# Kernel optimization log

Measured on AMD Instinct MI355X. Metric: run time of the kernel, lower is better.

## Reference

```python
import jax, jax.numpy as jnp
import numpy as np

SOS_TOKEN = 1
B, H, V, T = 64, 1024, 32000, 40
INPUT_SIZE = 4096


def setup_inputs() -> dict:
    key = jax.random.key(0)
    ks = jax.random.split(key, 12)
    s = 1.0 / np.sqrt(H)
    return {
        "output": jax.random.normal(ks[0], (B, INPUT_SIZE), jnp.float32),
        "h0": jax.random.normal(ks[1], (1, B, H), jnp.float32),
        "c0": jax.random.normal(ks[2], (1, B, H), jnp.float32),
        "target_outputs": jax.random.randint(ks[3], (B, T), 0, V, jnp.int64),
        "target_lengths": jnp.full((B,), T, jnp.int64),
        "embed": jax.random.normal(ks[4], (V, H), jnp.float32),
        "w_ih": jax.random.uniform(ks[5], (4 * H, H), jnp.float32, -s, s),
        "w_hh": jax.random.uniform(ks[6], (4 * H, H), jnp.float32, -s, s),
        "b_ih": jax.random.uniform(ks[7], (4 * H,), jnp.float32, -s, s),
        "b_hh": jax.random.uniform(ks[8], (4 * H,), jnp.float32, -s, s),
        "w_out": jax.random.uniform(ks[9], (V, H), jnp.float32, -s, s),
        "b_out": jax.random.uniform(ks[10], (V,), jnp.float32, -s, s),
    }


def _lstm_cell(x, h, c, w_ih, w_hh, b_ih, b_hh):
    # PyTorch LSTMCell math; gate order i, f, g, o
    gates = x @ w_ih.T + b_ih + h @ w_hh.T + b_hh  # [B, 4H]
    i, f, g, o = jnp.split(gates, 4, axis=-1)
    c2 = jax.nn.sigmoid(f) * c + jax.nn.sigmoid(i) * jnp.tanh(g)
    h2 = jax.nn.sigmoid(o) * jnp.tanh(c2)
    return h2, c2


def reference(output, h0, c0, target_outputs, target_lengths,
              embed, w_ih, w_hh, b_ih, b_hh, w_out, b_out):
    batch = output.shape[0]
    max_lens = int(jnp.max(target_lengths))
    h, c = h0[0], c0[0]  # num_layers=1 -> [B, H]

    # Initial symbol = SOS; initial dec_o = W(embed(SOS)) (no LSTM), as in torch code
    symbol0 = jnp.full((batch,), SOS_TOKEN, dtype=target_outputs.dtype)
    dec_o0 = embed[symbol0] @ w_out.T + b_out  # [B, V]

    def step(carry, _):
        symbol, dec_o, h, c = carry
        # emit current (symbol, dec_o), then decode next
        x = embed[symbol]  # [B, H]
        h2, c2 = _lstm_cell(x, h, c, w_ih, w_hh, b_ih, b_hh)
        dec2 = h2 @ w_out.T + b_out  # [B, V]
        sym2 = jnp.argmax(dec2, axis=-1).astype(symbol.dtype)  # greedy topk(1)
        return (sym2, dec2, h2, c2), (symbol, dec_o)
    (_, _, _, _), (symbols, decs) = jax.lax.scan(
        step, (symbol0, dec_o0, h, c), None, length=max_lens)

    decoder_outs = jnp.transpose(decs, (1, 0, 2))  # [B, T, V]
    symbol_outs = jnp.transpose(symbols, (1, 0))   # [B, T]
    return decoder_outs, symbol_outs
```

## Files before the change

### kernel.cpp

```cpp
#include <hip/hip_runtime.h>

#define Bdim 64
#define Hdim 1024
#define Vdim 32000
#define Tdim 40

typedef __bf16 bf16x8 __attribute__((ext_vector_type(8)));
typedef float  f32x4  __attribute__((ext_vector_type(4)));
typedef unsigned short u16x8 __attribute__((ext_vector_type(8)));
static_assert(sizeof(bf16x8) == 16, "bf16x8 must be 16B");

__device__ __forceinline__ unsigned long long pack_key(float f, int v) {
    unsigned u = __float_as_uint(f);
    u = (u & 0x80000000u) ? ~u : (u | 0x80000000u);
    return ((unsigned long long)u << 32) | (unsigned long long)(0xFFFFFFFFu - (unsigned)v);
}

__device__ __forceinline__ int decode_key(unsigned long long key) {
    return (int)(0xFFFFFFFFu - (unsigned)(key & 0xFFFFFFFFull));
}

__device__ __forceinline__ void gll16(const void* g, void* l) {
    __builtin_amdgcn_global_load_lds(
        (const __attribute__((address_space(1))) void*)g,
        (__attribute__((address_space(3))) void*)l, 16, 0, 0);
}

struct BSplit2 { unsigned short h, m; };

__device__ __forceinline__ BSplit2 bsplit2v(float x) {
    __bf16 h = (__bf16)x;  float r = x - (float)h;
    __bf16 m = (__bf16)r;
    BSplit2 s;
    s.h = __builtin_bit_cast(unsigned short, h);
    s.m = __builtin_bit_cast(unsigned short, m);
    return s;
}

__device__ __forceinline__ void bsplit2(float x, unsigned short& a, unsigned short& b) {
    BSplit2 s = bsplit2v(x);
    a = s.h; b = s.m;
}

template<int NW, int NCH, bool ARGMAX, bool BIAS, bool GATHER, bool NTST>
__device__ __forceinline__ void mm_core(
    unsigned char* sm,
    unsigned long long (*red)[4][16],
    const float* __restrict__ W,
    const unsigned short* __restrict__ Ah,
    const unsigned short* __restrict__ Am,
    const float* __restrict__ Gsrc,
    const unsigned long long* __restrict__ slots_in, int tstep,
    float* __restrict__ sym_dst,
    int n0, const float* __restrict__ bias,
    float* __restrict__ out, size_t out_bstride,
    unsigned long long* __restrict__ slots_out)
{
    constexpr int NT     = NW * 64;
    constexpr int WBYTES = NW * 2048;
    constexpr int BUFSZ  = WBYTES + 8192;

    const int tid  = threadIdx.x;
    const int lane = tid & 63;
    const int wid  = tid >> 6;

    f32x4 acc[4] = {};

    const unsigned char* Wb = (const unsigned char*)W;
    const unsigned char* Apb[2] = {(const unsigned char*)Ah, (const unsigned char*)Am};

    const int ar = tid >> 2, as = tid & 3;
    const int aswz = as ^ ((ar >> 1) & 3);
    const size_t asrc_off = (size_t)ar * 2048 + (size_t)aswz * 16;
    const size_t aldst    = (size_t)ar * 64 + (size_t)aswz * 16;

    const float* grow = nullptr;
    if constexpr (GATHER) {
        if (tid < 256) {
            int symv = 1;
            if (tstep > 0) {
                unsigned long long key = slots_in[ar];
                symv = decode_key(key);
                if (sym_dst != nullptr && as == 0)
                    sym_dst[ar * Tdim + tstep] = (float)symv;
            }
            grow = Gsrc + (size_t)symv * 1024 + as * 8;
        }
    }

    auto stage = [&](int bufidx, int ch) {
        unsigned char* bb = sm + bufidx * BUFSZ;
        const size_t kb4 = (size_t)ch * 128;
#pragma unroll
        for (int s = 0; s < 2; s++) {
            int gg = tid + NT * s;
            int rw = gg >> 3, cc = gg & 7;
            int sg = cc ^ (rw & 7);
            gll16(Wb + (size_t)rw * 4096 + kb4 + (size_t)sg * 16,
                  bb + ((wid * 64 + NT * s) << 4));
        }
        if constexpr (GATHER) {
            if (tid < 256) {
                const float* p = grow + ch * 32;
                float4 f0 = *(const float4*)(p);
                float4 f1 = *(const float4*)(p + 4);
                u16x8 vh, vm;
                BSplit2 s0 = bsplit2v(f0.x); vh[0] = s0.h; vm[0] = s0.m;
                BSplit2 s1 = bsplit2v(f0.y); vh[1] = s1.h; vm[1] = s1.m;
                BSplit2 s2 = bsplit2v(f0.z); vh[2] = s2.h; vm[2] = s2.m;
                BSplit2 s3 = bsplit2v(f0.w); vh[3] = s3.h; vm[3] = s3.m;
                BSplit2 s4 = bsplit2v(f1.x); vh[4] = s4.h; vm[4] = s4.m;
                BSplit2 s5 = bsplit2v(f1.y); vh[5] = s5.h; vm[5] = s5.m;
                BSplit2 s6 = bsplit2v(f1.z); vh[6] = s6.h; vm[6] = s6.m;
                BSplit2 s7 = bsplit2v(f1.w); vh[7] = s7.h; vm[7] = s7.m;
                *(u16x8*)(bb + WBYTES + aldst)        = vh;
                *(u16x8*)(bb + WBYTES + 4096 + aldst) = vm;
            }
        } else {
            if (tid < 256) {
                const size_t kb2 = (size_t)ch * 64;
#pragma unroll
                for (int pl = 0; pl < 2; pl++)
                    gll16(Apb[pl] + asrc_off + kb2,
                          bb + WBYTES + pl * 4096 + (wid << 10));
            }
        }
    };

    stage(0, 0);
    __syncthreads();

    const int col  = lane & 15;
    const int kg   = lane >> 4;
    const int wrow = wid * 16 + col;
    const int wg0  = (2 * kg) ^ (wrow & 7);
    const int wg1  = (2 * kg + 1) ^ (wrow & 7);

#pragma unroll 2
    for (int ch = 0; ch < NCH; ch++) {
        if (ch + 1 < NCH) stage((ch + 1) & 1, ch + 1);
        unsigned char* base = sm + (ch & 1) * BUFSZ;

        const unsigned char* Wr = base + wrow * 128;
        f32x4 w0 = *(const f32x4*)(Wr + (wg0 << 4));
        f32x4 w1 = *(const f32x4*)(Wr + (wg1 << 4));
        bf16x8 whi, wmid;
#pragma unroll
        for (int j = 0; j < 4; j++) {
            float x0 = w0[j], x1 = w1[j];
            __bf16 a0 = (__bf16)x0; float r0 = x0 - (float)a0;
            whi[j] = a0; wmid[j] = (__bf16)r0;
            __bf16 a1 = (__bf16)x1; float r1 = x1 - (float)a1;
            whi[4 + j] = a1; wmid[4 + j] = (__bf16)r1;
        }
#pragma unroll
        for (int bt = 0; bt < 4; bt++) {
            const int arow = bt * 16 + col;
            const unsigned char* Ar = base + WBYTES + arow * 64
                                    + ((kg ^ ((arow >> 1) & 3)) << 4);
            bf16x8 ahi = *(const bf16x8*)Ar;
            bf16x8 ami = *(const bf16x8*)(Ar + 4096);
            acc[bt] = __builtin_amdgcn_mfma_f32_16x16x32_bf16(whi,  ahi, acc[bt], 0, 0, 0);
            acc[bt] = __builtin_amdgcn_mfma_f32_16x16x32_bf16(whi,  ami, acc[bt], 0, 0, 0);
            acc[bt] = __builtin_amdgcn_mfma_f32_16x16x32_bf16(wmid, ahi, acc[bt], 0, 0, 0);
        }
        __syncthreads();
    }

    const int ncol = n0 + wid * 16 + kg * 4;
    f32x4 bv = {};
    if (BIAS) bv = *(const f32x4*)(bias + ncol);

    unsigned long long bk[4];
#pragma unroll
    for (int bt = 0; bt < 4; bt++) {
        const int b = bt * 16 + col;
        float* op = out + (size_t)b * out_bstride + ncol;
        f32x4 vv;
        unsigned long long best = 0ull;
#pragma unroll
        for (int r = 0; r < 4; r++) {
            float val = acc[bt][r];
            if (BIAS) val += bv[r];
            vv[r] = val;
            if (ARGMAX) {
                unsigned long long key = pack_key(val, ncol + r);
                if (key > best) best = key;
            }
        }
        if constexpr (NTST)
            __builtin_nontemporal_store(vv, (f32x4*)op);
        else
            *(f32x4*)op = vv;
        bk[bt] = best;
    }

    if constexpr (ARGMAX) {
#pragma unroll
        for (int bt = 0; bt < 4; bt++) {
            unsigned long long k = bk[bt];
            unsigned long long o = __shfl_xor(k, 16, 64); if (o > k) k = o;
            o = __shfl_xor(k, 32, 64);                    if (o > k) k = o;
            if (lane < 16) red[wid][bt][lane] = k;
        }
        __syncthreads();
        if (tid < 64) {
            const int bt = tid >> 4, c = tid & 15;
            unsigned long long k = red[0][bt][c];
#pragma unroll
            for (int w = 1; w < NW; w++)
                if (red[w][bt][c] > k) k = red[w][bt][c];
            atomicMax(&slots_out[bt * 16 + c], k);
        }
    }
}

template<bool AM>
__global__ __launch_bounds__(512, 1) void k_logits(
    const float* __restrict__ w_out,
    const unsigned short* __restrict__ ah, const unsigned short* __restrict__ am,
    const float* __restrict__ b_out, float* __restrict__ out,
    unsigned long long* __restrict__ slots)
{
    __shared__ __align__(16) unsigned char smem[2][24576];
    __shared__ unsigned long long red[8][4][16];
    const int vb = blockIdx.x * 128;
    mm_core<8, 32, AM, true, false, true>(&smem[0][0], red,
        w_out + (size_t)vb * Hdim, ah, am, nullptr, nullptr, 0, nullptr,
        vb, b_out, out, (size_t)Tdim * Vdim, slots);
}

__global__ __launch_bounds__(256, 2) void k_gates(
    const float* __restrict__ w_ih, const float* __restrict__ w_hh,
    const unsigned short* __restrict__ hh, const unsigned short* __restrict__ hm,
    const float* __restrict__ embed, unsigned long long* __restrict__ slots,
    int t, float* __restrict__ sym_out, float* __restrict__ gp)
{
    __shared__ __align__(16) unsigned char smem[2][16384];
    const int nbi = blockIdx.x, y = blockIdx.y, z = blockIdx.z;
    const float* W = (y ? w_hh : w_ih) + (size_t)nbi * 65536 + z * 256;
    float* gout = gp + (size_t)(y * 4 + z) * (Bdim * 4096);
    if (y)
        mm_core<4, 8, false, false, false, false>(&smem[0][0], nullptr, W,
            hh + z * 256, hm + z * 256, nullptr, nullptr, t, nullptr,
            nbi * 64, nullptr, gout, 4096, nullptr);
    else
        mm_core<4, 8, false, false, true, false>(&smem[0][0], nullptr, W,
            nullptr, nullptr, embed + z * 256, slots, t,
            ((nbi == 0 && z == 0) ? sym_out : nullptr),
            nbi * 64, nullptr, gout, 4096, nullptr);
}

__global__ void k_cell(const float* __restrict__ gp, const float* __restrict__ b_ih,
                       const float* __restrict__ b_hh, float* __restrict__ cbuf,
                       unsigned short* __restrict__ hh, unsigned short* __restrict__ hm,
                       unsigned long long* __restrict__ slots)
{
    const int idx = blockIdx.x * 256 + threadIdx.x;
    const int b = idx >> 10, k = idx & 1023;
    const size_t S = (size_t)Bdim * 4096;
    const size_t base = (size_t)b * 4096;
    float g[4];
#pragma unroll
    for (int q = 0; q < 4; q++) {
        size_t o = base + q * 1024 + k;
        float s = gp[o];
#pragma unroll
        for (int i = 1; i < 8; i++) s += gp[i * S + o];
        g[q] = s + b_ih[q * 1024 + k] + b_hh[q * 1024 + k];
    }
    float si = 1.f / (1.f + expf(-g[0]));
    float sf = 1.f / (1.f + expf(-g[1]));
    float so = 1.f / (1.f + expf(-g[3]));
    float c  = cbuf[idx];
    float c2 = sf * c + si * tanhf(g[2]);
    float h2 = so * tanhf(c2);
    cbuf[idx] = c2;
    unsigned short hs, ms;
    bsplit2(h2, hs, ms);
    const size_t o = (size_t)b * 1024 + k;
    hh[o] = hs; hm[o] = ms;
    if (idx < 64) slots[idx] = 0ull;
}

__global__ void k_init(const float* __restrict__ embed, const float* __restrict__ h0,
                       const float* __restrict__ c0,
                       unsigned short* __restrict__ xsh, unsigned short* __restrict__ xsm,
                       unsigned short* __restrict__ hh, unsigned short* __restrict__ hm,
                       float* __restrict__ cbuf, float* __restrict__ sym_out,
                       unsigned long long* __restrict__ slots)
{
    const int b = blockIdx.x, t4 = threadIdx.x * 4;
    if (threadIdx.x == 0) { sym_out[b * Tdim] = 1.0f; slots[b] = 0ull; }
    const size_t o = (size_t)b * 1024 + t4;
    ushort4 hi4, mi4;

    float4 e = *(const float4*)(embed + 1024 + t4);
    bsplit2(e.x, hi4.x, mi4.x);
    bsplit2(e.y, hi4.y, mi4.y);
    bsplit2(e.z, hi4.z, mi4.z);
    bsplit2(e.w, hi4.w, mi4.w);
    *(ushort4*)(xsh + o) = hi4; *(ushort4*)(xsm + o) = mi4;

    float4 hv = *(const float4*)(h0 + (size_t)b * 1024 + t4);
    bsplit2(hv.x, hi4.x, mi4.x);
    bsplit2(hv.y, hi4.y, mi4.y);
    bsplit2(hv.z, hi4.z, mi4.z);
    bsplit2(hv.w, hi4.w, mi4.w);
    *(ushort4*)(hh + o) = hi4; *(ushort4*)(hm + o) = mi4;

    float4 cv = *(const float4*)(c0 + (size_t)b * 1024 + t4);
    *(float4*)(cbuf + (size_t)b * 1024 + t4) = cv;
}

__global__ void k_symfinal(const unsigned long long* __restrict__ slots,
                           float* __restrict__ sym_out)
{
    const int b = threadIdx.x;
    sym_out[b * Tdim + (Tdim - 1)] = (float)decode_key(slots[b]);
}

extern "C" void kernel_launch(void* const* d_in, const int* in_sizes, int n_in,
                              void* d_out, int out_size, void* d_ws, size_t ws_size,
                              hipStream_t stream)
{
    const float* h0    = (const float*)d_in[1];
    const float* c0    = (const float*)d_in[2];
    const float* embed = (const float*)d_in[5];
    const float* w_ih  = (const float*)d_in[6];
    const float* w_hh  = (const float*)d_in[7];
    const float* b_ih  = (const float*)d_in[8];
    const float* b_hh  = (const float*)d_in[9];
    const float* w_out = (const float*)d_in[10];
    const float* b_out = (const float*)d_in[11];

    float* out = (float*)d_out;
    float* sym_out = out + (size_t)Bdim * Tdim * Vdim;

    unsigned short* hh  = (unsigned short*)d_ws;
    unsigned short* hm  = hh + (size_t)Bdim * 1024;
    unsigned short* xsh = hm + (size_t)Bdim * 1024;
    unsigned short* xsm = xsh + (size_t)Bdim * 1024;
    float* cbuf = (float*)(xsm + (size_t)Bdim * 1024);
    float* gp   = cbuf + (size_t)Bdim * Hdim;
    unsigned long long* slots = (unsigned long long*)(gp + 8ull * Bdim * 4096);

    k_init<<<Bdim, 256, 0, stream>>>(embed, h0, c0, xsh, xsm,
                                     hh, hm, cbuf, sym_out, slots);

    k_logits<false><<<Vdim / 128, 512, 0, stream>>>(w_out, xsh, xsm,
                                                    b_out, out, slots);

    for (int t = 0; t < Tdim - 1; t++) {
        k_gates<<<dim3(64, 2, 4), 256, 0, stream>>>(w_ih, w_hh, hh, hm,
                                                    embed, slots, t, sym_out, gp);
        k_cell<<<Bdim * Hdim / 256, 256, 0, stream>>>(gp, b_ih, b_hh, cbuf,
                                                      hh, hm, slots);
        k_logits<true><<<Vdim / 128, 512, 0, stream>>>(w_out, hh, hm,
                                                       b_out, out + (size_t)(t + 1) * Vdim,
                                                       slots);
    }
    k_symfinal<<<1, 64, 0, stream>>>(slots, sym_out);
}
```

Before: 2.271 ms.

## Fuse next-step h@W_hh gate matmul into logits kernel launch

The recurrent h@W_hh^T product for the next step now runs inside the same launch as the output logits projection, using 32 extra blocks that each cover 128 gate rows over the full K. The gate kernel only computes the embedding @ W_ih part, and the cell kernel sums 5 partial buffers instead of 8. This shortens the per-step critical path and fills the logits grid (250 blocks) with more work. Launch bounds rise to 4 waves per SIMD, which may constrain registers for the logits path.

```diff
diff --git a/kernel.cpp b/kernel.cpp
--- a/kernel.cpp
+++ b/kernel.cpp
@@ -216,39 +216,41 @@
 }
 
 template<bool AM>
-__global__ __launch_bounds__(512, 1) void k_logits(
-    const float* __restrict__ w_out,
-    const unsigned short* __restrict__ ah, const unsigned short* __restrict__ am,
-    const float* __restrict__ b_out, float* __restrict__ out,
-    unsigned long long* __restrict__ slots)
+__global__ __launch_bounds__(512, 4) void k_combined(
+    const float* __restrict__ w_out, const float* __restrict__ w_hh,
+    const unsigned short* __restrict__ la_h, const unsigned short* __restrict__ la_m,
+    const unsigned short* __restrict__ ga_h, const unsigned short* __restrict__ ga_m,
+    const float* __restrict__ b_out, float* __restrict__ dec_out,
+    float* __restrict__ gp0, unsigned long long* __restrict__ slots, int nhh)
 {
     __shared__ __align__(16) unsigned char smem[2][24576];
     __shared__ unsigned long long red[8][4][16];
-    const int vb = blockIdx.x * 128;
-    mm_core<8, 32, AM, true, false, true>(&smem[0][0], red,
-        w_out + (size_t)vb * Hdim, ah, am, nullptr, nullptr, 0, nullptr,
-        vb, b_out, out, (size_t)Tdim * Vdim, slots);
-}
-
-__global__ __launch_bounds__(256, 2) void k_gates(
-    const float* __restrict__ w_ih, const float* __restrict__ w_hh,
-    const unsigned short* __restrict__ hh, const unsigned short* __restrict__ hm,
-    const float* __restrict__ embed, unsigned long long* __restrict__ slots,
-    int t, float* __restrict__ sym_out, float* __restrict__ gp)
+    const int bid = blockIdx.x;
+    if (bid < nhh) {
+        mm_core<8, 32, false, false, false, false>(&smem[0][0], red,
+            w_hh + (size_t)bid * 131072, ga_h, ga_m, nullptr, nullptr, 0, nullptr,
+            bid * 128, nullptr, gp0, 4096, nullptr);
+    } else {
+        const int vb = (bid - nhh) * 128;
+        mm_core<8, 32, AM, true, false, true>(&smem[0][0], red,
+            w_out + (size_t)vb * Hdim, la_h, la_m, nullptr, nullptr, 0, nullptr,
+            vb, b_out, dec_out, (size_t)Tdim * Vdim, slots);
+    }
+}
+
+__global__ __launch_bounds__(256, 2) void k_gates_ih(
+    const float* __restrict__ w_ih, const float* __restrict__ embed,
+    unsigned long long* __restrict__ slots, int t,
+    float* __restrict__ sym_out, float* __restrict__ gp)
 {
     __shared__ __align__(16) unsigned char smem[2][16384];
-    const int nbi = blockIdx.x, y = blockIdx.y, z = blockIdx.z;
-    const float* W = (y ? w_hh : w_ih) + (size_t)nbi * 65536 + z * 256;
-    float* gout = gp + (size_t)(y * 4 + z) * (Bdim * 4096);
-    if (y)
-        mm_core<4, 8, false, false, false, false>(&smem[0][0], nullptr, W,
-            hh + z * 256, hm + z * 256, nullptr, nullptr, t, nullptr,
-            nbi * 64, nullptr, gout, 4096, nullptr);
-    else
-        mm_core<4, 8, false, false, true, false>(&smem[0][0], nullptr, W,
-            nullptr, nullptr, embed + z * 256, slots, t,
-            ((nbi == 0 && z == 0) ? sym_out : nullptr),
-            nbi * 64, nullptr, gout, 4096, nullptr);
+    const int nbi = blockIdx.x, z = blockIdx.y;
+    const float* W = w_ih + (size_t)nbi * 65536 + z * 256;
+    float* gout = gp + (size_t)(1 + z) * (Bdim * 4096);
+    mm_core<4, 8, false, false, true, false>(&smem[0][0], nullptr, W,
+        nullptr, nullptr, embed + z * 256, slots, t,
+        ((nbi == 0 && z == 0) ? sym_out : nullptr),
+        nbi * 64, nullptr, gout, 4096, nullptr);
 }
 
 __global__ void k_cell(const float* __restrict__ gp, const float* __restrict__ b_ih,
@@ -266,7 +268,7 @@
         size_t o = base + q * 1024 + k;
         float s = gp[o];
 #pragma unroll
-        for (int i = 1; i < 8; i++) s += gp[i * S + o];
+        for (int i = 1; i < 5; i++) s += gp[i * S + o];
         g[q] = s + b_ih[q * 1024 + k] + b_hh[q * 1024 + k];
     }
     float si = 1.f / (1.f + expf(-g[0]));
@@ -343,22 +345,23 @@
     unsigned short* xsm = xsh + (size_t)Bdim * 1024;
     float* cbuf = (float*)(xsm + (size_t)Bdim * 1024);
     float* gp   = cbuf + (size_t)Bdim * Hdim;
-    unsigned long long* slots = (unsigned long long*)(gp + 8ull * Bdim * 4096);
+    unsigned long long* slots = (unsigned long long*)(gp + 5ull * Bdim * 4096);
 
     k_init<<<Bdim, 256, 0, stream>>>(embed, h0, c0, xsh, xsm,
                                      hh, hm, cbuf, sym_out, slots);
 
-    k_logits<false><<<Vdim / 128, 512, 0, stream>>>(w_out, xsh, xsm,
-                                                    b_out, out, slots);
+    k_combined<false><<<282, 512, 0, stream>>>(w_out, w_hh, xsh, xsm, hh, hm,
+                                               b_out, out, gp, slots, 32);
 
     for (int t = 0; t < Tdim - 1; t++) {
-        k_gates<<<dim3(64, 2, 4), 256, 0, stream>>>(w_ih, w_hh, hh, hm,
-                                                    embed, slots, t, sym_out, gp);
+        k_gates_ih<<<dim3(64, 4), 256, 0, stream>>>(w_ih, embed, slots, t,
+                                                    sym_out, gp);
         k_cell<<<Bdim * Hdim / 256, 256, 0, stream>>>(gp, b_ih, b_hh, cbuf,
                                                       hh, hm, slots);
-        k_logits<true><<<Vdim / 128, 512, 0, stream>>>(w_out, hh, hm,
-                                                       b_out, out + (size_t)(t + 1) * Vdim,
-                                                       slots);
+        const int nhh = (t + 1 < Tdim - 1) ? 32 : 0;
+        k_combined<true><<<250 + nhh, 512, 0, stream>>>(w_out, w_hh, hh, hm, hh, hm,
+                                                        b_out, out + (size_t)(t + 1) * Vdim,
+                                                        gp, slots, nhh);
     }
     k_symfinal<<<1, 64, 0, stream>>>(slots, sym_out);
 }
```

Result: no change. 2.282 ms (+0.5%).
